# Kernel tuning notes

Hardware: AMD Instinct MI355X
Metric: run time of the kernel (lower is better)

## Reference

```python
import jax, jax.numpy as jnp
import numpy as np

B, T, D, H = 4, 2048, 1024, 16
DK = D // H


def setup_inputs() -> dict:
    key = jax.random.key(0)
    ks = jax.random.split(key, 9)
    s = 1.0 / np.sqrt(D)
    x = jax.random.normal(ks[0], (B, T, D), dtype=jnp.float32)
    # causal mask: 1 = keep, 0 = masked (broadcastable over batch and heads)
    mask = jnp.tril(jnp.ones((T, T), dtype=jnp.int32))[None, None]
    params = {}
    for i, name in enumerate(['Wq', 'Wk', 'Wv', 'Wo']):
        params[name] = jax.random.normal(ks[1 + i], (D, D), dtype=jnp.float32) * s
    for i, name in enumerate(['bq', 'bk', 'bv', 'bo']):
        params[name] = jax.random.normal(ks[5 + i], (D,), dtype=jnp.float32) * s
    return {'x': x, 'mask': mask, **params}


def reference(x, mask, Wq, Wk, Wv, Wo, bq, bk, bv, bo):
    Bn, Tn, Dn = x.shape
    # torch.nn.Linear: y = x @ W.T + b
    q = (x @ Wq.T + bq).reshape(Bn, Tn, H, DK).transpose(0, 2, 1, 3)  # [B,H,T,dk]
    k = (x @ Wk.T + bk).reshape(Bn, Tn, H, DK).transpose(0, 2, 1, 3)
    v = (x @ Wv.T + bv).reshape(Bn, Tn, H, DK).transpose(0, 2, 1, 3)
    scores = jnp.einsum('bhqd,bhkd->bhqk', q, k) / jnp.sqrt(jnp.float32(DK))
    scores = jnp.where(mask == 0, -jnp.inf, scores)
    attn = jax.nn.softmax(scores, axis=-1)
    out = jnp.einsum('bhqk,bhkd->bhqd', attn, v)  # [B,H,T,dk]
    out = out.transpose(0, 2, 1, 3).reshape(Bn, Tn, Dn)
    return out @ Wo.T + bo
```

## Files before the change

kernel.cpp:

```cpp
#include <hip/hip_runtime.h>
#include <hip/hip_bf16.h>

#define T_LEN 2048
#define D_DIM 1024
#define H_NUM 16
#define DK 64

typedef unsigned short u16;
typedef __bf16 bf16x8 __attribute__((ext_vector_type(8)));
typedef float f32x4 __attribute__((ext_vector_type(4)));
typedef u16 u16x8 __attribute__((ext_vector_type(8)));
typedef u16 u16x4 __attribute__((ext_vector_type(4)));

#define AS1 __attribute__((address_space(1)))
#define AS3 __attribute__((address_space(3)))

#define QSCALE 0.18033688011112042f

__device__ __forceinline__ u16 f2bf(float f) {
    unsigned u = __builtin_bit_cast(unsigned, f);
    unsigned rounding = 0x7FFFu + ((u >> 16) & 1u);
    return (u16)((u + rounding) >> 16);
}

__global__ __launch_bounds__(256) void cvt_bf16(const float* __restrict__ in,
                                                u16* __restrict__ out, int n8) {
    int i = blockIdx.x * blockDim.x + threadIdx.x;
    if (i >= n8) return;
    const float4* p = (const float4*)in + (size_t)i * 2;
    float4 a = p[0], b = p[1];
    u16x8 r;
    r[0] = f2bf(a.x); r[1] = f2bf(a.y); r[2] = f2bf(a.z); r[3] = f2bf(a.w);
    r[4] = f2bf(b.x); r[5] = f2bf(b.y); r[6] = f2bf(b.z); r[7] = f2bf(b.w);
    *((u16x8*)out + i) = r;
}

__global__ __launch_bounds__(256) void cvt4_bf16(const float* __restrict__ a,
                                                 const float* __restrict__ b,
                                                 const float* __restrict__ c,
                                                 const float* __restrict__ d,
                                                 u16* __restrict__ out, int n8per) {
    int s = blockIdx.y;
    const float* src = s == 0 ? a : (s == 1 ? b : (s == 2 ? c : d));
    int i = blockIdx.x * blockDim.x + threadIdx.x;
    if (i >= n8per) return;
    const float4* p = (const float4*)src + (size_t)i * 2;
    float4 x = p[0], y = p[1];
    u16x8 r;
    r[0] = f2bf(x.x); r[1] = f2bf(x.y); r[2] = f2bf(x.z); r[3] = f2bf(x.w);
    r[4] = f2bf(y.x); r[5] = f2bf(y.y); r[6] = f2bf(y.z); r[7] = f2bf(y.w);
    *((u16x8*)(out + (size_t)s * n8per * 8) + i) = r;
}

__global__ __launch_bounds__(512) void gemm_qkv(const u16* __restrict__ A,
                                                const u16* __restrict__ W,
                                                const float* __restrict__ b0,
                                                const float* __restrict__ b1,
                                                const float* __restrict__ b2,
                                                u16* __restrict__ Cout) {
    __shared__ u16 L[2][4][8192];
    const int tid = threadIdx.x, w = tid >> 6, lane = tid & 63;
    const int sw = (blockIdx.x & 7) * 48 + (blockIdx.x >> 3);
    const int xm = sw / 12, yn = sw % 12;
    const int tm = xm * 256, tn = yn * 256;
    const int wr = w >> 2, wc = w & 3;
    const int g = lane >> 4, ccol = lane & 15;
    const int gsw = (g ^ ((ccol >> 1) & 3)) * 8;
    const int K = 1024, NT = 16;

    const u16* Ab = A + (size_t)tm * K;
    const u16* Wb = W + (size_t)tn * K;

    const int srow = w * 16 + (lane >> 2);
    const int skk  = (((lane & 3) ^ ((lane >> 3) & 3))) * 8;

    f32x4 acc[8][4] = {};

    auto stage = [&](const u16* gb, int k0, int ksub, u16* reg) {
#pragma unroll
        for (int h2 = 0; h2 < 2; ++h2) {
            __builtin_amdgcn_global_load_lds(
                (AS1 const void*)(gb + (size_t)(h2 * 128 + srow) * K + k0 + ksub * 32 + skk),
                (AS3 void*)(reg + h2 * 4096 + w * 512), 16, 0, 0);
        }
    };

    stage(Ab, 0, 0, L[0][0]);
    stage(Wb, 0, 0, L[0][2]);
    stage(Ab, 0, 1, L[0][1]);
    stage(Wb, 0, 1, L[0][3]);
    stage(Ab, 64, 0, L[1][0]);
    stage(Wb, 64, 0, L[1][2]);
    asm volatile("s_waitcnt vmcnt(4)" ::: "memory");
    __builtin_amdgcn_s_barrier();

    bf16x8 bfr[4];
    for (int t = 0; t < NT; ++t) {
        const int par = t & 1;
        u16* LA0 = L[par][0]; u16* LA1 = L[par][1];
        u16* LB0 = L[par][2]; u16* LB1 = L[par][3];
#pragma unroll
        for (int p = 0; p < 4; ++p) {
            const int mh = (p & 1) * 4;
            u16* LAk = (p >> 1) ? LA1 : LA0;
            u16* LBk = (p >> 1) ? LB1 : LB0;
            bf16x8 af[4];
#pragma unroll
            for (int i = 0; i < 4; ++i)
                af[i] = *(const bf16x8*)(LAk + (wr * 128 + (mh + i) * 16 + ccol) * 32 + gsw);
            if ((p & 1) == 0) {
#pragma unroll
                for (int i = 0; i < 4; ++i)
                    bfr[i] = *(const bf16x8*)(LBk + (wc * 64 + i * 16 + ccol) * 32 + gsw);
            }
            if (p == 0)      { if (t + 1 < NT) stage(Ab, (t + 1) * 64, 1, L[(t + 1) & 1][1]); }
            else if (p == 1) { if (t + 1 < NT) stage(Wb, (t + 1) * 64, 1, L[(t + 1) & 1][3]); }
            else if (p == 2) { if (t + 2 < NT) stage(Ab, (t + 2) * 64, 0, L[par][0]); }
            else {
                if (t + 2 < NT) stage(Wb, (t + 2) * 64, 0, L[par][2]);
                if (t < NT - 2) asm volatile("s_waitcnt vmcnt(4)" ::: "memory");
                else            asm volatile("s_waitcnt vmcnt(0)" ::: "memory");
            }
            __builtin_amdgcn_s_barrier();
            asm volatile("s_waitcnt lgkmcnt(0)" ::: "memory");
            __builtin_amdgcn_sched_barrier(0);
            __builtin_amdgcn_s_setprio(1);
#pragma unroll
            for (int ni = 0; ni < 4; ++ni)
#pragma unroll
                for (int mi = 0; mi < 4; ++mi)
                    acc[mh + mi][ni] = __builtin_amdgcn_mfma_f32_16x16x32_bf16(
                        af[mi], bfr[ni], acc[mh + mi][ni], 0, 0, 0);
            __builtin_amdgcn_s_setprio(0);
            __builtin_amdgcn_s_barrier();
        }
    }

    const int mtx = yn >> 2;
    const float* bp = mtx == 0 ? b0 : (mtx == 1 ? b1 : b2);
#pragma unroll
    for (int mi = 0; mi < 8; ++mi) {
#pragma unroll
        for (int ni = 0; ni < 4; ++ni) {
            int nn = (tn + wc * 64 + ni * 16 + ccol) & 1023;
            float bv = bp[nn];
            int h = nn >> 6, d = nn & 63;
#pragma unroll
            for (int r = 0; r < 4; ++r) {
                int m = tm + wr * 128 + mi * 16 + g * 4 + r;
                float val = acc[mi][ni][r] + bv;
                if (mtx == 0) val *= QSCALE;
                int b = m >> 11, tt = m & (T_LEN - 1);
                Cout[(size_t)mtx * 8388608 +
                     ((size_t)(b * H_NUM + h) * T_LEN + tt) * DK + d] = f2bf(val);
            }
        }
    }
}

__global__ __launch_bounds__(256) void gemm_bt(const u16* __restrict__ A,
                                               const u16* __restrict__ W,
                                               const float* __restrict__ b0,
                                               float* __restrict__ Cout,
                                               int M, int N, int K,
                                               int nxt, int nyt) {
    __shared__ u16 lA[2][128 * 32];
    __shared__ u16 lB[2][128 * 32];
    const int tid = threadIdx.x;
    const int w = tid >> 6, lane = tid & 63;

    const int bid = blockIdx.x;
    const int idx = bid >> 3;
    const int y = idx % nyt;
    const int x = (bid & 7) * (nxt >> 3) + idx / nyt;
    const int tm = x * 128;
    const int tn = y * 128;

    const int wm = (w >> 1) * 64, wn = (w & 1) * 64;
    const int kgrp = (lane >> 4) * 8;

    f32x4 acc[4][4] = {};

    auto stage = [&](int buf, int k0) {
#pragma unroll
        for (int r = 0; r < 2; ++r) {
            int c = r * 256 + tid;
            int row = c >> 2, col = (c & 3) * 8;
            __builtin_amdgcn_global_load_lds(
                (AS1 const void*)(A + (size_t)(tm + row) * K + k0 + col),
                (AS3 void*)(&lA[buf][(r * 256 + w * 64) * 8]), 16, 0, 0);
            __builtin_amdgcn_global_load_lds(
                (AS1 const void*)(W + (size_t)(tn + row) * K + k0 + col),
                (AS3 void*)(&lB[buf][(r * 256 + w * 64) * 8]), 16, 0, 0);
        }
    };

    stage(0, 0);
    asm volatile("s_waitcnt vmcnt(0)" ::: "memory");
    __syncthreads();

    const int niter = K >> 5;
    for (int it = 0; it < niter; ++it) {
        const int cur = it & 1;
        if (it + 1 < niter) stage(cur ^ 1, (it + 1) << 5);

        bf16x8 af[4], bfr[4];
#pragma unroll
        for (int i = 0; i < 4; ++i) {
            af[i]  = *(const bf16x8*)(&lA[cur][(wm + i * 16 + (lane & 15)) * 32 + kgrp]);
            bfr[i] = *(const bf16x8*)(&lB[cur][(wn + i * 16 + (lane & 15)) * 32 + kgrp]);
        }
#pragma unroll
        for (int mi = 0; mi < 4; ++mi)
#pragma unroll
            for (int ni = 0; ni < 4; ++ni)
                acc[mi][ni] = __builtin_amdgcn_mfma_f32_16x16x32_bf16(
                    af[mi], bfr[ni], acc[mi][ni], 0, 0, 0);

        asm volatile("s_waitcnt vmcnt(0)" ::: "memory");
        __syncthreads();
    }

    const int crow0 = (lane >> 4) * 4;
    const int ccol = lane & 15;
#pragma unroll
    for (int mi = 0; mi < 4; ++mi) {
#pragma unroll
        for (int ni = 0; ni < 4; ++ni) {
            int n = tn + wn + ni * 16 + ccol;
            float bv = b0[n & 1023];
#pragma unroll
            for (int r = 0; r < 4; ++r) {
                int m = tm + wm + mi * 16 + crow0 + r;
                Cout[(size_t)m * N + n] = acc[mi][ni][r] + bv;
            }
        }
    }
}

__global__ __launch_bounds__(512) void attn_fwd(const u16* __restrict__ q,
                                                const u16* __restrict__ k,
                                                const u16* __restrict__ v,
                                                u16* __restrict__ o) {
    __shared__ u16 lK[2][64 * 64];
    __shared__ u16 lV[2][64 * 64];
    __shared__ u16 lP[8][16 * 72];
    __shared__ float lSc[8][16];

    const int tid = threadIdx.x, w = tid >> 6, lane = tid & 63;
    const int bid = blockIdx.x;
    const int idx = bid >> 3;
    const int bh = (bid & 7) * 8 + (idx & 7);
    const int bx = idx >> 3;

    const u16* qb = q + (size_t)bh * T_LEN * DK;
    const u16* kb = k + (size_t)bh * T_LEN * DK;
    const u16* vb = v + (size_t)bh * T_LEN * DK;

    const int g = lane >> 4;
    const int ccol = lane & 15;
    const int kg = tid >> 4;
    const int dc = tid & 15;
    const int wk = w - 4;
    const int b_ = bh >> 4, h_ = bh & 15;

    for (int seg = 0; seg < 2; ++seg) {
        const int qblk = seg ? (15 - bx) : bx;
        const int q0 = qblk * 128;
        const int ntiles = 2 * qblk + 2;
        const int rowbase = q0 + w * 16;
        const int myq = rowbase + ccol;

        bf16x8 qa[2];
#pragma unroll
        for (int kk = 0; kk < 2; ++kk)
            qa[kk] = *(const bf16x8*)(qb + (size_t)(rowbase + ccol) * DK + kk * 32 + g * 8);

        f32x4 oacc[4] = {};
        float mrow = -1e30f, lpart = 0.f;

        u16x4 vr[4];
        if (w >= 4) {
#pragma unroll
            for (int r2 = 0; r2 < 2; ++r2) {
                int c = r2 * 256 + wk * 64 + lane;
                int row = c >> 3, ch = c & 7;
                __builtin_amdgcn_global_load_lds(
                    (AS1 const void*)(kb + (size_t)row * DK + (ch ^ (row & 7)) * 8),
                    (AS3 void*)(&lK[0][(r2 * 256 + wk * 64) * 8]), 16, 0, 0);
            }
        } else {
#pragma unroll
            for (int i = 0; i < 4; ++i)
                vr[i] = *(const u16x4*)(vb + (size_t)(kg * 4 + i) * DK + dc * 4);
        }

        for (int kt = 0; kt < ntiles; ++kt) {
            const int bf = kt & 1;
            const int kv0 = kt << 6;
            asm volatile("s_waitcnt vmcnt(0)" ::: "memory");
            if (w < 4) {
#pragma unroll
                for (int j = 0; j < 4; ++j) {
                    int d = dc * 4 + j;
                    u16x4 t4;
                    t4[0] = vr[0][j]; t4[1] = vr[1][j]; t4[2] = vr[2][j]; t4[3] = vr[3][j];
                    *(u16x4*)(&lV[bf][d * 64 +
                        (((kg >> 1) ^ ((d >> 1) & 7)) * 8 + (kg & 1) * 4)]) = t4;
                }
            }
            __syncthreads();

            if (kt + 1 < ntiles) {
                const int kvn = (kt + 1) << 6;
                if (w >= 4) {
#pragma unroll
                    for (int r2 = 0; r2 < 2; ++r2) {
                        int c = r2 * 256 + wk * 64 + lane;
                        int row = c >> 3, ch = c & 7;
                        __builtin_amdgcn_global_load_lds(
                            (AS1 const void*)(kb + (size_t)(kvn + row) * DK + (ch ^ (row & 7)) * 8),
                            (AS3 void*)(&lK[bf ^ 1][(r2 * 256 + wk * 64) * 8]), 16, 0, 0);
                    }
                } else {
#pragma unroll
                    for (int i = 0; i < 4; ++i)
                        vr[i] = *(const u16x4*)(vb + (size_t)(kvn + kg * 4 + i) * DK + dc * 4);
                }
            }

            if (kv0 < rowbase + 16) {
                f32x4 sacc[4] = {};
                __builtin_amdgcn_s_setprio(1);
#pragma unroll
                for (int nt = 0; nt < 4; ++nt)
#pragma unroll
                    for (int kk = 0; kk < 2; ++kk) {
                        bf16x8 kf = *(const bf16x8*)(&lK[bf][(nt * 16 + ccol) * 64 +
                                                     (((kk * 4 + g) ^ (ccol & 7)) * 8)]);
                        sacc[nt] = __builtin_amdgcn_mfma_f32_16x16x32_bf16(
                            kf, qa[kk], sacc[nt], 0, 0, 0);
                    }
                __builtin_amdgcn_s_setprio(0);

                const bool full = (kv0 + 63) <= rowbase;
                float mx = -1e30f;
#pragma unroll
                for (int nt = 0; nt < 4; ++nt)
#pragma unroll
                    for (int r = 0; r < 4; ++r) {
                        float sv = sacc[nt][r];
                        if (!full && (kv0 + nt * 16 + g * 4 + r > myq)) sv = -1e30f;
                        sacc[nt][r] = sv;
                        mx = fmaxf(mx, sv);
                    }
                mx = fmaxf(mx, __shfl_xor(mx, 16));
                mx = fmaxf(mx, __shfl_xor(mx, 32));

                const bool skiprow = (mx <= mrow + 8.f);
                float mnew = skiprow ? mrow : mx;
                float p[4][4];
                float rsl = 0.f;
#pragma unroll
                for (int nt = 0; nt < 4; ++nt)
#pragma unroll
                    for (int r = 0; r < 4; ++r) {
                        float pv = __builtin_amdgcn_exp2f(sacc[nt][r] - mnew);
                        p[nt][r] = pv;
                        rsl += pv;
                    }
                float scal = skiprow ? 1.f : __builtin_amdgcn_exp2f(mrow - mnew);
                lpart = lpart * scal + rsl;
                mrow = mnew;

                if (lane < 16) lSc[w][lane] = scal;
#pragma unroll
                for (int nt = 0; nt < 4; ++nt) {
                    u16x4 t4;
                    t4[0] = f2bf(p[nt][0]); t4[1] = f2bf(p[nt][1]);
                    t4[2] = f2bf(p[nt][2]); t4[3] = f2bf(p[nt][3]);
                    *(u16x4*)(&lP[w][ccol * 72 + nt * 16 + g * 4]) = t4;
                }
                asm volatile("s_waitcnt lgkmcnt(0)" ::: "memory");

                f32x4 scalC = *(const f32x4*)(&lSc[w][g * 4]);
                if (__any(!skiprow)) {
#pragma unroll
                    for (int nt2 = 0; nt2 < 4; ++nt2)
#pragma unroll
                        for (int r = 0; r < 4; ++r) oacc[nt2][r] *= scalC[r];
                }

                bf16x8 pa[2];
#pragma unroll
                for (int kk2 = 0; kk2 < 2; ++kk2)
                    pa[kk2] = *(const bf16x8*)(&lP[w][ccol * 72 + kk2 * 32 + g * 8]);

                const int vsw = (ccol >> 1) & 7;
                __builtin_amdgcn_s_setprio(1);
#pragma unroll
                for (int nt2 = 0; nt2 < 4; ++nt2) {
#pragma unroll
                    for (int kk2 = 0; kk2 < 2; ++kk2) {
                        bf16x8 vf = *(const bf16x8*)(&lV[bf][(nt2 * 16 + ccol) * 64 +
                                                     (((kk2 * 4 + g) ^ vsw) * 8)]);
                        oacc[nt2] = __builtin_amdgcn_mfma_f32_16x16x32_bf16(
                            pa[kk2], vf, oacc[nt2], 0, 0, 0);
                    }
                }
                __builtin_amdgcn_s_setprio(0);
            }
        }
        __syncthreads();

        float rs = lpart;
        rs += __shfl_xor(rs, 16);
        rs += __shfl_xor(rs, 32);
        if (lane < 16) lSc[w][lane] = rs;
        asm volatile("s_waitcnt lgkmcnt(0)" ::: "memory");
        f32x4 rsC = *(const f32x4*)(&lSc[w][g * 4]);
#pragma unroll
        for (int r = 0; r < 4; ++r) {
            float inv = 1.0f / rsC[r];
            int trow = rowbase + g * 4 + r;
#pragma unroll
            for (int nt2 = 0; nt2 < 4; ++nt2) {
                float val = oacc[nt2][r] * inv;
                o[(size_t)(b_ * T_LEN + trow) * D_DIM + h_ * DK + nt2 * 16 + ccol] = f2bf(val);
            }
        }
        __syncthreads();
    }
}

extern "C" void kernel_launch(void* const* d_in, const int* in_sizes, int n_in,
                              void* d_out, int out_size, void* d_ws, size_t ws_size,
                              hipStream_t stream) {
    const float* x  = (const float*)d_in[0];
    const float* Wq = (const float*)d_in[2];
    const float* Wk = (const float*)d_in[3];
    const float* Wv = (const float*)d_in[4];
    const float* Wo = (const float*)d_in[5];
    const float* bq = (const float*)d_in[6];
    const float* bk = (const float*)d_in[7];
    const float* bv = (const float*)d_in[8];
    const float* bo = (const float*)d_in[9];

    char* ws = (char*)d_ws;
    u16* xb   = (u16*)(ws);
    u16* wqb  = (u16*)(ws + 16777216);
    u16* wob  = (u16*)(ws + 23068672);
    u16* qws  = (u16*)(ws + 25165824);
    u16* kws  = (u16*)(ws + 41943040);
    u16* vws  = (u16*)(ws + 58720256);
    u16* attnb = xb;

    cvt_bf16<<<4096, 256, 0, stream>>>(x, xb, 1048576);
    cvt4_bf16<<<dim3(512, 4), 256, 0, stream>>>(Wq, Wk, Wv, Wo, wqb, 131072);

    gemm_qkv<<<384, 512, 0, stream>>>(xb, wqb, bq, bk, bv, qws);

    attn_fwd<<<512, 512, 0, stream>>>(qws, kws, vws, attnb);

    gemm_bt<<<512, 256, 0, stream>>>(attnb, wob, bo, (float*)d_out, 8192, 1024, 1024, 64, 8);
}
```

Baseline: 273.5 us.

## Retile QKV GEMM to 256x192 tiles for 512 blocks

Changes the fused QKV projection GEMM tile from 256x256 to 256x192, so the grid grows from 384 to 512 blocks. The aim is to fill all compute units evenly (384 blocks leave a partial second wave on a 256-CU part). Staging for the B operand is rewritten with an uneven thread split, and because a tile can now straddle the Q/K/V boundary, the epilogue picks the bias per 16-column sub-tile. Each block does less work per load, lowering data reuse, and the B staging uses only half the threads for its second load.

Result: slower. 294.8 us (+7.8%).

```diff
diff --git a/kernel.cpp b/kernel.cpp
--- a/kernel.cpp
+++ b/kernel.cpp
@@ -52,72 +52,81 @@
     *((u16x8*)(out + (size_t)s * n8per * 8) + i) = r;
 }
 
-__global__ __launch_bounds__(512) void gemm_qkv(const u16* __restrict__ A,
-                                                const u16* __restrict__ W,
-                                                const float* __restrict__ b0,
-                                                const float* __restrict__ b1,
-                                                const float* __restrict__ b2,
-                                                u16* __restrict__ Cout) {
-    __shared__ u16 L[2][4][8192];
+__global__ __launch_bounds__(512) void gemm_qkv192(const u16* __restrict__ A,
+                                                   const u16* __restrict__ W,
+                                                   const float* __restrict__ b0,
+                                                   const float* __restrict__ b1,
+                                                   const float* __restrict__ b2,
+                                                   u16* __restrict__ Cout) {
+    __shared__ u16 LA[2][2][8192];
+    __shared__ u16 LB[2][2][6144];
     const int tid = threadIdx.x, w = tid >> 6, lane = tid & 63;
-    const int sw = (blockIdx.x & 7) * 48 + (blockIdx.x >> 3);
-    const int xm = sw / 12, yn = sw % 12;
-    const int tm = xm * 256, tn = yn * 256;
+    const int sw = (blockIdx.x & 7) * 64 + (blockIdx.x >> 3);
+    const int xm = sw >> 4, yn = sw & 15;
+    const int tm = xm * 256, tn = yn * 192;
     const int wr = w >> 2, wc = w & 3;
     const int g = lane >> 4, ccol = lane & 15;
     const int gsw = (g ^ ((ccol >> 1) & 3)) * 8;
-    const int K = 1024, NT = 16;
-
-    const u16* Ab = A + (size_t)tm * K;
-    const u16* Wb = W + (size_t)tn * K;
-
-    const int srow = w * 16 + (lane >> 2);
-    const int skk  = (((lane & 3) ^ ((lane >> 3) & 3))) * 8;
-
-    f32x4 acc[8][4] = {};
-
-    auto stage = [&](const u16* gb, int k0, int ksub, u16* reg) {
-#pragma unroll
-        for (int h2 = 0; h2 < 2; ++h2) {
+    const int NT = 16;
+
+    f32x4 acc[8][3] = {};
+
+    auto stageA = [&](u16* dst, int kcol) {
+#pragma unroll
+        for (int h = 0; h < 2; ++h) {
+            int c = h * 512 + tid;
+            int row = c >> 2;
+            int kc = ((c & 3) ^ ((row >> 1) & 3)) * 8;
             __builtin_amdgcn_global_load_lds(
-                (AS1 const void*)(gb + (size_t)(h2 * 128 + srow) * K + k0 + ksub * 32 + skk),
-                (AS3 void*)(reg + h2 * 4096 + w * 512), 16, 0, 0);
+                (AS1 const void*)(A + (size_t)(tm + row) * 1024 + kcol + kc),
+                (AS3 void*)(dst + h * 4096 + w * 512), 16, 0, 0);
         }
     };
-
-    stage(Ab, 0, 0, L[0][0]);
-    stage(Wb, 0, 0, L[0][2]);
-    stage(Ab, 0, 1, L[0][1]);
-    stage(Wb, 0, 1, L[0][3]);
-    stage(Ab, 64, 0, L[1][0]);
-    stage(Wb, 64, 0, L[1][2]);
+    auto stageB = [&](u16* dst, int kcol) {
+        {
+            int c = tid, row = c >> 2;
+            int kc = ((c & 3) ^ ((row >> 1) & 3)) * 8;
+            __builtin_amdgcn_global_load_lds(
+                (AS1 const void*)(W + (size_t)(tn + row) * 1024 + kcol + kc),
+                (AS3 void*)(dst + w * 512), 16, 0, 0);
+        }
+        {
+            int c = 512 + (tid & 255), row = c >> 2;
+            int kc = ((c & 3) ^ ((row >> 1) & 3)) * 8;
+            __builtin_amdgcn_global_load_lds(
+                (AS1 const void*)(W + (size_t)(tn + row) * 1024 + kcol + kc),
+                (AS3 void*)(dst + 4096 + (w & 3) * 512), 16, 0, 0);
+        }
+    };
+
+    stageA(LA[0][0], 0);  stageB(LB[0][0], 0);
+    stageA(LA[0][1], 32); stageB(LB[0][1], 32);
+    stageA(LA[1][0], 64); stageB(LB[1][0], 64);
     asm volatile("s_waitcnt vmcnt(4)" ::: "memory");
     __builtin_amdgcn_s_barrier();
 
-    bf16x8 bfr[4];
+    bf16x8 bfr[3];
     for (int t = 0; t < NT; ++t) {
         const int par = t & 1;
-        u16* LA0 = L[par][0]; u16* LA1 = L[par][1];
-        u16* LB0 = L[par][2]; u16* LB1 = L[par][3];
 #pragma unroll
         for (int p = 0; p < 4; ++p) {
-            const int mh = (p & 1) * 4;
-            u16* LAk = (p >> 1) ? LA1 : LA0;
-            u16* LBk = (p >> 1) ? LB1 : LB0;
+            const int kk = p >> 1, mh = (p & 1) * 4;
+            const u16* LAp = LA[par][kk];
+            const u16* LBp = LB[par][kk];
             bf16x8 af[4];
 #pragma unroll
             for (int i = 0; i < 4; ++i)
-                af[i] = *(const bf16x8*)(LAk + (wr * 128 + (mh + i) * 16 + ccol) * 32 + gsw);
+                af[i] = *(const bf16x8*)(LAp + (wr * 128 + (mh + i) * 16 + ccol) * 32 + gsw);
             if ((p & 1) == 0) {
 #pragma unroll
-                for (int i = 0; i < 4; ++i)
-                    bfr[i] = *(const bf16x8*)(LBk + (wc * 64 + i * 16 + ccol) * 32 + gsw);
-            }
-            if (p == 0)      { if (t + 1 < NT) stage(Ab, (t + 1) * 64, 1, L[(t + 1) & 1][1]); }
-            else if (p == 1) { if (t + 1 < NT) stage(Wb, (t + 1) * 64, 1, L[(t + 1) & 1][3]); }
-            else if (p == 2) { if (t + 2 < NT) stage(Ab, (t + 2) * 64, 0, L[par][0]); }
+                for (int i = 0; i < 3; ++i)
+                    bfr[i] = *(const bf16x8*)(LBp + (wc * 48 + i * 16 + ccol) * 32 + gsw);
+            }
+            if (p == 0)      { if (t + 1 < NT) stageA(LA[par ^ 1][1], (t + 1) * 64 + 32); }
+            else if (p == 1) { if (t + 1 < NT) stageB(LB[par ^ 1][1], (t + 1) * 64 + 32); }
+            else if (p == 2) { if (t + 2 < NT) stageA(LA[par][0], (t + 2) * 64); }
             else {
-                if (t + 2 < NT) stage(Wb, (t + 2) * 64, 0, L[par][2]);
+                if (t + 2 < NT) stageB(LB[par][0], (t + 2) * 64);
                 if (t < NT - 2) asm volatile("s_waitcnt vmcnt(4)" ::: "memory");
                 else            asm volatile("s_waitcnt vmcnt(0)" ::: "memory");
             }
@@ -126,9 +135,9 @@
             __builtin_amdgcn_sched_barrier(0);
             __builtin_amdgcn_s_setprio(1);
 #pragma unroll
-            for (int ni = 0; ni < 4; ++ni)
-#pragma unroll
-                for (int mi = 0; mi < 4; ++mi)
+            for (int mi = 0; mi < 4; ++mi)
+#pragma unroll
+                for (int ni = 0; ni < 3; ++ni)
                     acc[mh + mi][ni] = __builtin_amdgcn_mfma_f32_16x16x32_bf16(
                         af[mi], bfr[ni], acc[mh + mi][ni], 0, 0, 0);
             __builtin_amdgcn_s_setprio(0);
@@ -136,15 +145,16 @@
         }
     }
 
-    const int mtx = yn >> 2;
-    const float* bp = mtx == 0 ? b0 : (mtx == 1 ? b1 : b2);
-#pragma unroll
-    for (int mi = 0; mi < 8; ++mi) {
-#pragma unroll
-        for (int ni = 0; ni < 4; ++ni) {
-            int nn = (tn + wc * 64 + ni * 16 + ccol) & 1023;
-            float bv = bp[nn];
-            int h = nn >> 6, d = nn & 63;
+#pragma unroll
+    for (int ni = 0; ni < 3; ++ni) {
+        const int n0 = tn + wc * 48 + ni * 16;
+        const int mtx = n0 >> 10;
+        const float* bp = mtx == 0 ? b0 : (mtx == 1 ? b1 : b2);
+        const int nn = (n0 + ccol) & 1023;
+        const float bv = bp[nn];
+        const int h = nn >> 6, d = nn & 63;
+#pragma unroll
+        for (int mi = 0; mi < 8; ++mi) {
 #pragma unroll
             for (int r = 0; r < 4; ++r) {
                 int m = tm + wr * 128 + mi * 16 + g * 4 + r;
@@ -458,7 +468,7 @@
     cvt_bf16<<<4096, 256, 0, stream>>>(x, xb, 1048576);
     cvt4_bf16<<<dim3(512, 4), 256, 0, stream>>>(Wq, Wk, Wv, Wo, wqb, 131072);
 
-    gemm_qkv<<<384, 512, 0, stream>>>(xb, wqb, bq, bk, bv, qws);
+    gemm_qkv192<<<512, 512, 0, stream>>>(xb, wqb, bq, bk, bv, qws);
 
     attn_fwd<<<512, 512, 0, stream>>>(qws, kws, vws, attnb);
 
```

## Rewrite output projection GEMM with deeper pipelined swizzled LDS and merge convert kernels

Applied to the files above, without the earlier changes.

Replaces the generic 128x128 output-projection GEMM with a 256x128-tile, 512-thread kernel. It uses a triple-stage, half-K-step LDS pipeline with XOR-swizzled layout, vmcnt-based partial waits, and raised priority around MFMA blocks. The x and weight conversion kernels are also merged into a single launch. The aim is to hide global load latency, cut LDS bank conflicts and drop one launch. In exchange it uses more shared memory per block and fewer, larger blocks (256).

After: 273.5 us. Within noise of the previous version (-0.0%).

```diff
diff --git a/kernel.cpp b/kernel.cpp
--- a/kernel.cpp
+++ b/kernel.cpp
@@ -23,33 +23,28 @@
     return (u16)((u + rounding) >> 16);
 }
 
-__global__ __launch_bounds__(256) void cvt_bf16(const float* __restrict__ in,
-                                                u16* __restrict__ out, int n8) {
-    int i = blockIdx.x * blockDim.x + threadIdx.x;
-    if (i >= n8) return;
-    const float4* p = (const float4*)in + (size_t)i * 2;
+__global__ __launch_bounds__(256) void cvt_all(const float* __restrict__ x,
+                                               const float* __restrict__ wq,
+                                               const float* __restrict__ wk,
+                                               const float* __restrict__ wv,
+                                               const float* __restrict__ wo,
+                                               u16* __restrict__ xb,
+                                               u16* __restrict__ wb) {
+    int i = blockIdx.x * 256 + threadIdx.x;
+    const float* src; u16* dst; int off;
+    if (i < 1048576) { src = x; dst = xb; off = i; }
+    else {
+        int j = i - 1048576;
+        int s = j >> 17; off = j & 131071;
+        src = s == 0 ? wq : (s == 1 ? wk : (s == 2 ? wv : wo));
+        dst = wb + (size_t)s * 1048576;
+    }
+    const float4* p = (const float4*)src + (size_t)off * 2;
     float4 a = p[0], b = p[1];
     u16x8 r;
     r[0] = f2bf(a.x); r[1] = f2bf(a.y); r[2] = f2bf(a.z); r[3] = f2bf(a.w);
     r[4] = f2bf(b.x); r[5] = f2bf(b.y); r[6] = f2bf(b.z); r[7] = f2bf(b.w);
-    *((u16x8*)out + i) = r;
-}
-
-__global__ __launch_bounds__(256) void cvt4_bf16(const float* __restrict__ a,
-                                                 const float* __restrict__ b,
-                                                 const float* __restrict__ c,
-                                                 const float* __restrict__ d,
-                                                 u16* __restrict__ out, int n8per) {
-    int s = blockIdx.y;
-    const float* src = s == 0 ? a : (s == 1 ? b : (s == 2 ? c : d));
-    int i = blockIdx.x * blockDim.x + threadIdx.x;
-    if (i >= n8per) return;
-    const float4* p = (const float4*)src + (size_t)i * 2;
-    float4 x = p[0], y = p[1];
-    u16x8 r;
-    r[0] = f2bf(x.x); r[1] = f2bf(x.y); r[2] = f2bf(x.z); r[3] = f2bf(x.w);
-    r[4] = f2bf(y.x); r[5] = f2bf(y.y); r[6] = f2bf(y.z); r[7] = f2bf(y.w);
-    *((u16x8*)(out + (size_t)s * n8per * 8) + i) = r;
+    *((u16x8*)dst + off) = r;
 }
 
 __global__ __launch_bounds__(512) void gemm_qkv(const u16* __restrict__ A,
@@ -158,81 +153,94 @@
     }
 }
 
-__global__ __launch_bounds__(256) void gemm_bt(const u16* __restrict__ A,
-                                               const u16* __restrict__ W,
-                                               const float* __restrict__ b0,
-                                               float* __restrict__ Cout,
-                                               int M, int N, int K,
-                                               int nxt, int nyt) {
-    __shared__ u16 lA[2][128 * 32];
-    __shared__ u16 lB[2][128 * 32];
-    const int tid = threadIdx.x;
-    const int w = tid >> 6, lane = tid & 63;
-
-    const int bid = blockIdx.x;
-    const int idx = bid >> 3;
-    const int y = idx % nyt;
-    const int x = (bid & 7) * (nxt >> 3) + idx / nyt;
-    const int tm = x * 128;
-    const int tn = y * 128;
-
-    const int wm = (w >> 1) * 64, wn = (w & 1) * 64;
-    const int kgrp = (lane >> 4) * 8;
+__global__ __launch_bounds__(512) void gemm_o(const u16* __restrict__ A,
+                                              const u16* __restrict__ W,
+                                              const float* __restrict__ b0,
+                                              float* __restrict__ Cout) {
+    __shared__ u16 LA[2][2][8192];
+    __shared__ u16 LB[2][2][4096];
+    const int tid = threadIdx.x, w = tid >> 6, lane = tid & 63;
+    const int sw = (blockIdx.x & 7) * 32 + (blockIdx.x >> 3);
+    const int xm = sw >> 3, yn = sw & 7;
+    const int tm = xm * 256, tn = yn * 128;
+    const int wr = w >> 1, wc = w & 1;
+    const int g = lane >> 4, ccol = lane & 15;
+    const int gsw = (g ^ ((ccol >> 1) & 3)) * 8;
+    const int NT = 16;
 
     f32x4 acc[4][4] = {};
 
-    auto stage = [&](int buf, int k0) {
-#pragma unroll
-        for (int r = 0; r < 2; ++r) {
-            int c = r * 256 + tid;
-            int row = c >> 2, col = (c & 3) * 8;
+    auto stageA = [&](u16* dst, int kcol) {
+#pragma unroll
+        for (int h = 0; h < 2; ++h) {
+            int c = h * 512 + tid;
+            int row = c >> 2;
+            int kc = ((c & 3) ^ ((row >> 1) & 3)) * 8;
             __builtin_amdgcn_global_load_lds(
-                (AS1 const void*)(A + (size_t)(tm + row) * K + k0 + col),
-                (AS3 void*)(&lA[buf][(r * 256 + w * 64) * 8]), 16, 0, 0);
-            __builtin_amdgcn_global_load_lds(
-                (AS1 const void*)(W + (size_t)(tn + row) * K + k0 + col),
-                (AS3 void*)(&lB[buf][(r * 256 + w * 64) * 8]), 16, 0, 0);
+                (AS1 const void*)(A + (size_t)(tm + row) * 1024 + kcol + kc),
+                (AS3 void*)(dst + h * 4096 + w * 512), 16, 0, 0);
         }
     };
-
-    stage(0, 0);
-    asm volatile("s_waitcnt vmcnt(0)" ::: "memory");
-    __syncthreads();
-
-    const int niter = K >> 5;
-    for (int it = 0; it < niter; ++it) {
-        const int cur = it & 1;
-        if (it + 1 < niter) stage(cur ^ 1, (it + 1) << 5);
-
-        bf16x8 af[4], bfr[4];
-#pragma unroll
-        for (int i = 0; i < 4; ++i) {
-            af[i]  = *(const bf16x8*)(&lA[cur][(wm + i * 16 + (lane & 15)) * 32 + kgrp]);
-            bfr[i] = *(const bf16x8*)(&lB[cur][(wn + i * 16 + (lane & 15)) * 32 + kgrp]);
-        }
-#pragma unroll
-        for (int mi = 0; mi < 4; ++mi)
-#pragma unroll
-            for (int ni = 0; ni < 4; ++ni)
-                acc[mi][ni] = __builtin_amdgcn_mfma_f32_16x16x32_bf16(
-                    af[mi], bfr[ni], acc[mi][ni], 0, 0, 0);
-
-        asm volatile("s_waitcnt vmcnt(0)" ::: "memory");
-        __syncthreads();
-    }
-
-    const int crow0 = (lane >> 4) * 4;
-    const int ccol = lane & 15;
+    auto stageB = [&](u16* dst, int kcol) {
+        int row = tid >> 2;
+        int kc = ((tid & 3) ^ ((row >> 1) & 3)) * 8;
+        __builtin_amdgcn_global_load_lds(
+            (AS1 const void*)(W + (size_t)(tn + row) * 1024 + kcol + kc),
+            (AS3 void*)(dst + w * 512), 16, 0, 0);
+    };
+
+    stageA(LA[0][0], 0);  stageB(LB[0][0], 0);
+    stageA(LA[0][1], 32); stageB(LB[0][1], 32);
+    stageA(LA[1][0], 64); stageB(LB[1][0], 64);
+    asm volatile("s_waitcnt vmcnt(3)" ::: "memory");
+    __builtin_amdgcn_s_barrier();
+
+    for (int t = 0; t < NT; ++t) {
+        const int par = t & 1;
+#pragma unroll
+        for (int p = 0; p < 2; ++p) {
+            const u16* LAp = LA[par][p];
+            const u16* LBp = LB[par][p];
+            bf16x8 af[4], bfr[4];
+#pragma unroll
+            for (int i = 0; i < 4; ++i) {
+                af[i]  = *(const bf16x8*)(LAp + (wr * 64 + i * 16 + ccol) * 32 + gsw);
+                bfr[i] = *(const bf16x8*)(LBp + (wc * 64 + i * 16 + ccol) * 32 + gsw);
+            }
+            if (p == 0) {
+                if (t + 1 < NT) { stageA(LA[par ^ 1][1], (t + 1) * 64 + 32);
+                                  stageB(LB[par ^ 1][1], (t + 1) * 64 + 32); }
+            } else {
+                if (t + 2 < NT) { stageA(LA[par][0], (t + 2) * 64);
+                                  stageB(LB[par][0], (t + 2) * 64); }
+                if (t < NT - 2) asm volatile("s_waitcnt vmcnt(3)" ::: "memory");
+                else            asm volatile("s_waitcnt vmcnt(0)" ::: "memory");
+            }
+            __builtin_amdgcn_s_barrier();
+            asm volatile("s_waitcnt lgkmcnt(0)" ::: "memory");
+            __builtin_amdgcn_sched_barrier(0);
+            __builtin_amdgcn_s_setprio(1);
+#pragma unroll
+            for (int mi = 0; mi < 4; ++mi)
+#pragma unroll
+                for (int ni = 0; ni < 4; ++ni)
+                    acc[mi][ni] = __builtin_amdgcn_mfma_f32_16x16x32_bf16(
+                        af[mi], bfr[ni], acc[mi][ni], 0, 0, 0);
+            __builtin_amdgcn_s_setprio(0);
+            __builtin_amdgcn_s_barrier();
+        }
+    }
+
 #pragma unroll
     for (int mi = 0; mi < 4; ++mi) {
 #pragma unroll
         for (int ni = 0; ni < 4; ++ni) {
-            int n = tn + wn + ni * 16 + ccol;
-            float bv = b0[n & 1023];
+            int n = tn + wc * 64 + ni * 16 + ccol;
+            float bv = b0[n];
 #pragma unroll
             for (int r = 0; r < 4; ++r) {
-                int m = tm + wm + mi * 16 + crow0 + r;
-                Cout[(size_t)m * N + n] = acc[mi][ni][r] + bv;
+                int m = tm + wr * 64 + mi * 16 + g * 4 + r;
+                Cout[(size_t)m * 1024 + n] = acc[mi][ni][r] + bv;
             }
         }
     }
@@ -455,12 +463,11 @@
     u16* vws  = (u16*)(ws + 58720256);
     u16* attnb = xb;
 
-    cvt_bf16<<<4096, 256, 0, stream>>>(x, xb, 1048576);
-    cvt4_bf16<<<dim3(512, 4), 256, 0, stream>>>(Wq, Wk, Wv, Wo, wqb, 131072);
+    cvt_all<<<6144, 256, 0, stream>>>(x, Wq, Wk, Wv, Wo, xb, wqb);
 
     gemm_qkv<<<384, 512, 0, stream>>>(xb, wqb, bq, bk, bv, qws);
 
     attn_fwd<<<512, 512, 0, stream>>>(qws, kws, vws, attnb);
 
-    gemm_bt<<<512, 256, 0, stream>>>(attnb, wob, bo, (float*)d_out, 8192, 1024, 1024, 64, 8);
-}
+    gemm_o<<<256, 512, 0, stream>>>(attnb, wob, bo, (float*)d_out);
+}
```
